# Optimization experiments

Hardware: AMD Instinct MI355X
Metric: run time of the kernel (lower is better)

The kernel has to match this reference:

```python
import jax, jax.numpy as jnp
import numpy as np

WINDOW_SIZE = 32
SIM_THRESHOLD = 0.7
N_TOKENS = 262144
DIM = 256


def setup_inputs() -> dict:
    key = jax.random.key(0)
    x = jax.random.normal(key, (N_TOKENS, DIM), dtype=jnp.float32)
    return {"x": x}


def reference(x):
    """Stage 1 (global window pruning) + Stage 3 (sequential merge) of FocusModules.

    Returns:
      mask1: [N] bool keep-mask equivalent to compute_patch_similarity's index list
             (indices retained are exactly jnp.where(mask1)[0]).
      compressed: [N, D] float, features with stage-3-dropped tokens zeroed
             (mask-compacted form of spatial_token_compression's output; the
             retained rows in order equal the torch output).
    """
    N, D = x.shape
    W = WINDOW_SIZE
    nw = N // W  # N chosen as multiple of W

    # F.normalize(x, p=2, dim=-1) with eps clamp
    norms = jnp.maximum(jnp.linalg.norm(x, axis=-1, keepdims=True), 1e-12)
    xn = x / norms

    # ---- Stage 1: per-window cosine-similarity thresholding (vectorized over windows)
    win = xn.reshape(nw, W, D)
    sim = jnp.einsum('nwd,nvd->nwv', win, win)          # [nw, W, W]
    mean_sim = sim.mean(axis=2)                          # [nw, W]
    mu = mean_sim.mean(axis=1, keepdims=True)
    sd = mean_sim.std(axis=1, ddof=1, keepdims=True)     # torch .std() is unbiased
    keep = ~(mean_sim > (mu + sd))                       # [nw, W] bool
    # fallback: if a window keeps nothing, keep its argmin token
    any_kept = keep.any(axis=1, keepdims=True)
    fallback = jnp.arange(W)[None, :] == mean_sim.argmin(axis=1)[:, None]
    keep = jnp.where(any_kept, keep, fallback)
    mask1 = keep.reshape(N)

    # ---- Stage 3: adjacent-pair cosine similarity pruning
    sim_adj = jnp.sum(xn[:-1] * xn[1:], axis=-1)         # [N-1] (unit vectors -> dot = cosine)
    mask3 = jnp.concatenate([jnp.ones((1,), dtype=bool), sim_adj < SIM_THRESHOLD])
    compressed = x * mask3[:, None].astype(x.dtype)      # zeroed instead of compacted (jit-static shape)

    return mask1, compressed
```

## Files before the change

### kernel.cpp

```cpp
#include <hip/hip_runtime.h>
#include <math.h>

#define TOKW 32
#define DIMS 256

__global__ __launch_bounds__(256) void focus_kernel(
    const float* __restrict__ x,
    float* __restrict__ out_mask,
    float* __restrict__ out_comp)
{
    const int w   = blockIdx.x;
    const int tid = threadIdx.x;
    const int tok = tid >> 3;
    const int lt  = tid & 7;

    __shared__ float sh_xn[TOKW][DIMS];
    __shared__ float sh_prev[DIMS];
    __shared__ float sh_s[DIMS];
    __shared__ float sh_m[TOKW];

    const long long g0 = (long long)w * TOKW;
    const long long tokbase = (g0 + tok) * (DIMS / 4);
    const float4* xv = (const float4*)x;

    float4 v[8];
#pragma unroll
    for (int j = 0; j < 8; ++j)
        v[j] = xv[tokbase + lt + 8 * j];

    float ss = 0.f;
#pragma unroll
    for (int j = 0; j < 8; ++j)
        ss += v[j].x * v[j].x + v[j].y * v[j].y + v[j].z * v[j].z + v[j].w * v[j].w;
    ss += __shfl_xor(ss, 1);
    ss += __shfl_xor(ss, 2);
    ss += __shfl_xor(ss, 4);
    const float rn = 1.0f / fmaxf(sqrtf(ss), 1e-12f);

#pragma unroll
    for (int j = 0; j < 8; ++j) {
        float4 n4 = make_float4(v[j].x * rn, v[j].y * rn, v[j].z * rn, v[j].w * rn);
        *(float4*)&sh_xn[tok][4 * (lt + 8 * j)] = n4;
    }

    if (tid < 64) {
        float4 pv = make_float4(0.f, 0.f, 0.f, 0.f);
        if (w > 0) pv = xv[(g0 - 1) * (DIMS / 4) + tid];
        float ps = pv.x * pv.x + pv.y * pv.y + pv.z * pv.z + pv.w * pv.w;
        ps += __shfl_xor(ps, 1);
        ps += __shfl_xor(ps, 2);
        ps += __shfl_xor(ps, 4);
        ps += __shfl_xor(ps, 8);
        ps += __shfl_xor(ps, 16);
        ps += __shfl_xor(ps, 32);
        const float prn = 1.0f / fmaxf(sqrtf(ps), 1e-12f);
        *(float4*)&sh_prev[tid * 4] =
            make_float4(pv.x * prn, pv.y * prn, pv.z * prn, pv.w * prn);
    }

    __syncthreads();

    {
        float acc = 0.f;
#pragma unroll
        for (int t = 0; t < TOKW; ++t)
            acc += sh_xn[t][tid];
        sh_s[tid] = acc;
    }
    __syncthreads();

    {
        float dp = 0.f;
#pragma unroll
        for (int j = 0; j < 8; ++j) {
            float4 s4 = *(const float4*)&sh_s[4 * (lt + 8 * j)];
            dp += v[j].x * s4.x + v[j].y * s4.y + v[j].z * s4.z + v[j].w * s4.w;
        }
        dp += __shfl_xor(dp, 1);
        dp += __shfl_xor(dp, 2);
        dp += __shfl_xor(dp, 4);
        if (lt == 0) sh_m[tok] = dp * rn * (1.0f / 32.0f);
    }
    __syncthreads();

    float mu = 0.f;
#pragma unroll
    for (int t = 0; t < TOKW; ++t)
        mu += sh_m[t];
    mu *= (1.0f / 32.0f);

    float var = 0.f;
#pragma unroll
    for (int t = 0; t < TOKW; ++t) {
        float d = sh_m[t] - mu;
        var += d * d;
    }
    var *= (1.0f / 31.0f);
    const float thr = mu + sqrtf(var);

    int cnt = 0, amin = 0;
    float mmin = sh_m[0];
#pragma unroll
    for (int t = 0; t < TOKW; ++t) {
        float m = sh_m[t];
        cnt += (m <= thr) ? 1 : 0;
        if (m < mmin) { mmin = m; amin = t; }
    }

    if (tid < TOKW) {
        bool k = (cnt > 0) ? (sh_m[tid] <= thr) : (tid == amin);
        out_mask[g0 + tid] = k ? 1.0f : 0.0f;
    }

    const float* prevrow = (tok == 0) ? sh_prev : sh_xn[tok - 1];
    float ap = 0.f;
#pragma unroll
    for (int j = 0; j < 8; ++j) {
        float4 p4 = *(const float4*)&prevrow[4 * (lt + 8 * j)];
        ap += v[j].x * p4.x + v[j].y * p4.y + v[j].z * p4.z + v[j].w * p4.w;
    }
    ap += __shfl_xor(ap, 1);
    ap += __shfl_xor(ap, 2);
    ap += __shfl_xor(ap, 4);
    const float sim_adj = ap * rn;
    const float mult = (sim_adj < 0.7f) ? 1.0f : 0.0f;

    float4* ov = (float4*)out_comp;
#pragma unroll
    for (int j = 0; j < 8; ++j)
        ov[tokbase + lt + 8 * j] =
            make_float4(v[j].x * mult, v[j].y * mult, v[j].z * mult, v[j].w * mult);
}

extern "C" void kernel_launch(void* const* d_in, const int* in_sizes, int n_in,
                              void* d_out, int out_size, void* d_ws, size_t ws_size,
                              hipStream_t stream) {
    const float* x = (const float*)d_in[0];
    const int ND = in_sizes[0];
    const int N  = ND / DIMS;
    const int nw = N / TOKW;

    float* out_mask = (float*)d_out;
    float* out_comp = out_mask + N;

    focus_kernel<<<nw, 256, 0, stream>>>(x, out_mask, out_comp);
}
```

Before: 436.0 us.

## Replace shared-memory window staging with wave shuffles and nontemporal stores

```diff
diff --git a/kernel.cpp b/kernel.cpp
--- a/kernel.cpp
+++ b/kernel.cpp
@@ -3,20 +3,24 @@
 
 #define TOKW 32
 #define DIMS 256
+
+typedef float f4v __attribute__((ext_vector_type(4)));
 
 __global__ __launch_bounds__(256) void focus_kernel(
     const float* __restrict__ x,
     float* __restrict__ out_mask,
     float* __restrict__ out_comp)
 {
-    const int w   = blockIdx.x;
-    const int tid = threadIdx.x;
-    const int tok = tid >> 3;
-    const int lt  = tid & 7;
-
-    __shared__ float sh_xn[TOKW][DIMS];
-    __shared__ float sh_prev[DIMS];
-    __shared__ float sh_s[DIMS];
+    const int tid  = threadIdx.x;
+    const int w    = blockIdx.x;
+    const int tok  = tid >> 3;
+    const int lt   = tid & 7;
+    const int wid  = tid >> 6;
+    const int tw   = tok & 7;
+    const int lane = tid & 63;
+
+    __shared__ float sh_ws[4][DIMS];
+    __shared__ float sh_bd[5][DIMS];
     __shared__ float sh_m[TOKW];
 
     const long long g0 = (long long)w * TOKW;
@@ -27,6 +31,9 @@
 #pragma unroll
     for (int j = 0; j < 8; ++j)
         v[j] = xv[tokbase + lt + 8 * j];
+
+    float4 pv = make_float4(0.f, 0.f, 0.f, 0.f);
+    if (tid < 64 && w > 0) pv = xv[(g0 - 1) * (DIMS / 4) + tid];
 
     float ss = 0.f;
 #pragma unroll
@@ -37,15 +44,47 @@
     ss += __shfl_xor(ss, 4);
     const float rn = 1.0f / fmaxf(sqrtf(ss), 1e-12f);
 
-#pragma unroll
-    for (int j = 0; j < 8; ++j) {
-        float4 n4 = make_float4(v[j].x * rn, v[j].y * rn, v[j].z * rn, v[j].w * rn);
-        *(float4*)&sh_xn[tok][4 * (lt + 8 * j)] = n4;
+    float4 t[8];
+#pragma unroll
+    for (int j = 0; j < 8; ++j) {
+        t[j].x = v[j].x * rn; t[j].y = v[j].y * rn;
+        t[j].z = v[j].z * rn; t[j].w = v[j].w * rn;
+    }
+
+    if (tw == 7) {
+#pragma unroll
+        for (int j = 0; j < 8; ++j)
+            *(float4*)&sh_bd[wid][4 * (lt + 8 * j)] = t[j];
+    }
+
+#pragma unroll
+    for (int j = 0; j < 8; ++j) {
+        t[j].x += __shfl_xor(t[j].x, 8);
+        t[j].y += __shfl_xor(t[j].y, 8);
+        t[j].z += __shfl_xor(t[j].z, 8);
+        t[j].w += __shfl_xor(t[j].w, 8);
+    }
+#pragma unroll
+    for (int j = 0; j < 8; ++j) {
+        t[j].x += __shfl_xor(t[j].x, 16);
+        t[j].y += __shfl_xor(t[j].y, 16);
+        t[j].z += __shfl_xor(t[j].z, 16);
+        t[j].w += __shfl_xor(t[j].w, 16);
+    }
+#pragma unroll
+    for (int j = 0; j < 8; ++j) {
+        t[j].x += __shfl_xor(t[j].x, 32);
+        t[j].y += __shfl_xor(t[j].y, 32);
+        t[j].z += __shfl_xor(t[j].z, 32);
+        t[j].w += __shfl_xor(t[j].w, 32);
+    }
+    if (tw == 0) {
+#pragma unroll
+        for (int j = 0; j < 8; ++j)
+            *(float4*)&sh_ws[wid][4 * (lt + 8 * j)] = t[j];
     }
 
     if (tid < 64) {
-        float4 pv = make_float4(0.f, 0.f, 0.f, 0.f);
-        if (w > 0) pv = xv[(g0 - 1) * (DIMS / 4) + tid];
         float ps = pv.x * pv.x + pv.y * pv.y + pv.z * pv.z + pv.w * pv.w;
         ps += __shfl_xor(ps, 1);
         ps += __shfl_xor(ps, 2);
@@ -54,45 +93,67 @@
         ps += __shfl_xor(ps, 16);
         ps += __shfl_xor(ps, 32);
         const float prn = 1.0f / fmaxf(sqrtf(ps), 1e-12f);
-        *(float4*)&sh_prev[tid * 4] =
+        *(float4*)&sh_bd[4][tid * 4] =
             make_float4(pv.x * prn, pv.y * prn, pv.z * prn, pv.w * prn);
     }
 
-    __syncthreads();
-
-    {
-        float acc = 0.f;
-#pragma unroll
-        for (int t = 0; t < TOKW; ++t)
-            acc += sh_xn[t][tid];
-        sh_s[tid] = acc;
-    }
     __syncthreads();
 
     {
         float dp = 0.f;
 #pragma unroll
         for (int j = 0; j < 8; ++j) {
-            float4 s4 = *(const float4*)&sh_s[4 * (lt + 8 * j)];
-            dp += v[j].x * s4.x + v[j].y * s4.y + v[j].z * s4.z + v[j].w * s4.w;
+            const int f = 4 * (lt + 8 * j);
+            const float4 s0 = *(const float4*)&sh_ws[0][f];
+            const float4 s1 = *(const float4*)&sh_ws[1][f];
+            const float4 s2 = *(const float4*)&sh_ws[2][f];
+            const float4 s3 = *(const float4*)&sh_ws[3][f];
+            dp += v[j].x * (s0.x + s1.x + s2.x + s3.x)
+                + v[j].y * (s0.y + s1.y + s2.y + s3.y)
+                + v[j].z * (s0.z + s1.z + s2.z + s3.z)
+                + v[j].w * (s0.w + s1.w + s2.w + s3.w);
         }
         dp += __shfl_xor(dp, 1);
         dp += __shfl_xor(dp, 2);
         dp += __shfl_xor(dp, 4);
         if (lt == 0) sh_m[tok] = dp * rn * (1.0f / 32.0f);
     }
+
+    const float prn_s = __shfl(rn, (lane - 8) & 63);
+    float ap = 0.f;
+#pragma unroll
+    for (int j = 0; j < 8; ++j) {
+        const float px = __shfl(v[j].x, (lane - 8) & 63);
+        const float py = __shfl(v[j].y, (lane - 8) & 63);
+        const float pz = __shfl(v[j].z, (lane - 8) & 63);
+        const float pw = __shfl(v[j].w, (lane - 8) & 63);
+        ap += px * v[j].x + py * v[j].y + pz * v[j].z + pw * v[j].w;
+    }
+    float pscale = prn_s;
+
     __syncthreads();
 
+    if (tw == 0) {
+        const float* prow = (tok == 0) ? sh_bd[4] : sh_bd[wid - 1];
+        ap = 0.f;
+#pragma unroll
+        for (int j = 0; j < 8; ++j) {
+            const float4 p4 = *(const float4*)&prow[4 * (lt + 8 * j)];
+            ap += p4.x * v[j].x + p4.y * v[j].y + p4.z * v[j].z + p4.w * v[j].w;
+        }
+        pscale = 1.0f;
+    }
+
     float mu = 0.f;
 #pragma unroll
-    for (int t = 0; t < TOKW; ++t)
-        mu += sh_m[t];
+    for (int ti = 0; ti < TOKW; ++ti)
+        mu += sh_m[ti];
     mu *= (1.0f / 32.0f);
 
     float var = 0.f;
 #pragma unroll
-    for (int t = 0; t < TOKW; ++t) {
-        float d = sh_m[t] - mu;
+    for (int ti = 0; ti < TOKW; ++ti) {
+        float d = sh_m[ti] - mu;
         var += d * d;
     }
     var *= (1.0f / 31.0f);
@@ -101,35 +162,32 @@
     int cnt = 0, amin = 0;
     float mmin = sh_m[0];
 #pragma unroll
-    for (int t = 0; t < TOKW; ++t) {
-        float m = sh_m[t];
+    for (int ti = 0; ti < TOKW; ++ti) {
+        float m = sh_m[ti];
         cnt += (m <= thr) ? 1 : 0;
-        if (m < mmin) { mmin = m; amin = t; }
+        if (m < mmin) { mmin = m; amin = ti; }
     }
 
     if (tid < TOKW) {
         bool k = (cnt > 0) ? (sh_m[tid] <= thr) : (tid == amin);
-        out_mask[g0 + tid] = k ? 1.0f : 0.0f;
-    }
-
-    const float* prevrow = (tok == 0) ? sh_prev : sh_xn[tok - 1];
-    float ap = 0.f;
-#pragma unroll
-    for (int j = 0; j < 8; ++j) {
-        float4 p4 = *(const float4*)&prevrow[4 * (lt + 8 * j)];
-        ap += v[j].x * p4.x + v[j].y * p4.y + v[j].z * p4.z + v[j].w * p4.w;
-    }
-    ap += __shfl_xor(ap, 1);
-    ap += __shfl_xor(ap, 2);
-    ap += __shfl_xor(ap, 4);
-    const float sim_adj = ap * rn;
-    const float mult = (sim_adj < 0.7f) ? 1.0f : 0.0f;
-
-    float4* ov = (float4*)out_comp;
-#pragma unroll
-    for (int j = 0; j < 8; ++j)
-        ov[tokbase + lt + 8 * j] =
-            make_float4(v[j].x * mult, v[j].y * mult, v[j].z * mult, v[j].w * mult);
+        __builtin_nontemporal_store(k ? 1.0f : 0.0f, out_mask + g0 + tid);
+    }
+
+    float sim = ap;
+    sim += __shfl_xor(sim, 1);
+    sim += __shfl_xor(sim, 2);
+    sim += __shfl_xor(sim, 4);
+    sim *= rn * pscale;
+    const float mult = (sim < 0.7f) ? 1.0f : 0.0f;
+
+    f4v* ov = (f4v*)out_comp;
+#pragma unroll
+    for (int j = 0; j < 8; ++j) {
+        f4v o;
+        o.x = v[j].x * mult; o.y = v[j].y * mult;
+        o.z = v[j].z * mult; o.w = v[j].w * mult;
+        __builtin_nontemporal_store(o, ov + tokbase + lt + 8 * j);
+    }
 }
 
 extern "C" void kernel_launch(void* const* d_in, const int* in_sizes, int n_in,
```

Measured after the change: 451.5 us. +3.6%, slower.

## Process one window per wavefront with shuffle reductions, dropping shared memory

Applied to the files above, without the earlier changes.

```diff
diff --git a/kernel.cpp b/kernel.cpp
--- a/kernel.cpp
+++ b/kernel.cpp
@@ -3,133 +3,108 @@
 
 #define TOKW 32
 #define DIMS 256
+#define F4PT (DIMS / 4)
 
-__global__ __launch_bounds__(256) void focus_kernel(
+__global__ __launch_bounds__(256, 4) void focus_kernel(
     const float* __restrict__ x,
     float* __restrict__ out_mask,
     float* __restrict__ out_comp)
 {
-    const int w   = blockIdx.x;
-    const int tid = threadIdx.x;
-    const int tok = tid >> 3;
-    const int lt  = tid & 7;
+    const int tid  = threadIdx.x;
+    const int lane = tid & 63;
+    const int win  = blockIdx.x * 4 + (tid >> 6);
 
-    __shared__ float sh_xn[TOKW][DIMS];
-    __shared__ float sh_prev[DIMS];
-    __shared__ float sh_s[DIMS];
-    __shared__ float sh_m[TOKW];
+    const long long t0 = (long long)win * TOKW;
+    const long long b4 = t0 * F4PT;
+    const float4* xv = (const float4*)x;
+    float4* ov = (float4*)out_comp;
 
-    const long long g0 = (long long)w * TOKW;
-    const long long tokbase = (g0 + tok) * (DIMS / 4);
-    const float4* xv = (const float4*)x;
+    float4 rp = make_float4(0.f, 0.f, 0.f, 0.f);
+    if (win > 0) rp = xv[b4 - F4PT + lane];
 
-    float4 v[8];
+    float4 q[4];
+    q[0] = xv[b4 + 0 * F4PT + lane];
+    q[1] = xv[b4 + 1 * F4PT + lane];
+    q[2] = xv[b4 + 2 * F4PT + lane];
+    q[3] = xv[b4 + 3 * F4PT + lane];
+
+    float ssp = rp.x * rp.x + rp.y * rp.y + rp.z * rp.z + rp.w * rp.w;
 #pragma unroll
-    for (int j = 0; j < 8; ++j)
-        v[j] = xv[tokbase + lt + 8 * j];
+    for (int mm = 1; mm < 64; mm <<= 1) ssp += __shfl_xor(ssp, mm);
+    float rn_prev = 1.0f / fmaxf(sqrtf(ssp), 1e-12f);
 
-    float ss = 0.f;
-#pragma unroll
-    for (int j = 0; j < 8; ++j)
-        ss += v[j].x * v[j].x + v[j].y * v[j].y + v[j].z * v[j].z + v[j].w * v[j].w;
-    ss += __shfl_xor(ss, 1);
-    ss += __shfl_xor(ss, 2);
-    ss += __shfl_xor(ss, 4);
-    const float rn = 1.0f / fmaxf(sqrtf(ss), 1e-12f);
+    float4 s = make_float4(0.f, 0.f, 0.f, 0.f);
+    float rn[TOKW];
+    unsigned int simbits = 0;
 
 #pragma unroll
-    for (int j = 0; j < 8; ++j) {
-        float4 n4 = make_float4(v[j].x * rn, v[j].y * rn, v[j].z * rn, v[j].w * rn);
-        *(float4*)&sh_xn[tok][4 * (lt + 8 * j)] = n4;
+    for (int j = 0; j < TOKW; ++j) {
+        const float4 rc = q[j & 3];
+        if (j + 4 < TOKW) q[j & 3] = xv[b4 + (j + 4) * F4PT + lane];
+
+        float ss = rc.x * rc.x + rc.y * rc.y + rc.z * rc.z + rc.w * rc.w;
+        float dd = rc.x * rp.x + rc.y * rp.y + rc.z * rp.z + rc.w * rp.w;
+#pragma unroll
+        for (int mm = 1; mm < 64; mm <<= 1) {
+            ss += __shfl_xor(ss, mm);
+            dd += __shfl_xor(dd, mm);
+        }
+        const float r = 1.0f / fmaxf(sqrtf(ss), 1e-12f);
+        rn[j] = r;
+        const float sim = dd * r * rn_prev;
+        if (sim < 0.7f) simbits |= (1u << j);
+        s.x += rc.x * r; s.y += rc.y * r; s.z += rc.z * r; s.w += rc.w * r;
+        rn_prev = r;
+        rp = rc;
     }
 
-    if (tid < 64) {
-        float4 pv = make_float4(0.f, 0.f, 0.f, 0.f);
-        if (w > 0) pv = xv[(g0 - 1) * (DIMS / 4) + tid];
-        float ps = pv.x * pv.x + pv.y * pv.y + pv.z * pv.z + pv.w * pv.w;
-        ps += __shfl_xor(ps, 1);
-        ps += __shfl_xor(ps, 2);
-        ps += __shfl_xor(ps, 4);
-        ps += __shfl_xor(ps, 8);
-        ps += __shfl_xor(ps, 16);
-        ps += __shfl_xor(ps, 32);
-        const float prn = 1.0f / fmaxf(sqrtf(ps), 1e-12f);
-        *(float4*)&sh_prev[tid * 4] =
-            make_float4(pv.x * prn, pv.y * prn, pv.z * prn, pv.w * prn);
+    q[0] = xv[b4 + 0 * F4PT + lane];
+    q[1] = xv[b4 + 1 * F4PT + lane];
+    q[2] = xv[b4 + 2 * F4PT + lane];
+    q[3] = xv[b4 + 3 * F4PT + lane];
+
+    float m[TOKW];
+    float mlane = 0.f;
+#pragma unroll
+    for (int j = 0; j < TOKW; ++j) {
+        const float4 rc = q[j & 3];
+        if (j + 4 < TOKW) q[j & 3] = xv[b4 + (j + 4) * F4PT + lane];
+
+        float dp = rc.x * s.x + rc.y * s.y + rc.z * s.z + rc.w * s.w;
+#pragma unroll
+        for (int mm = 1; mm < 64; mm <<= 1) dp += __shfl_xor(dp, mm);
+        const float mj = dp * rn[j] * (1.0f / 32.0f);
+        m[j] = mj;
+        if (lane == j) mlane = mj;
+
+        const float mult = ((simbits >> j) & 1u) ? 1.0f : 0.0f;
+        ov[b4 + j * F4PT + lane] =
+            make_float4(rc.x * mult, rc.y * mult, rc.z * mult, rc.w * mult);
     }
-
-    __syncthreads();
-
-    {
-        float acc = 0.f;
-#pragma unroll
-        for (int t = 0; t < TOKW; ++t)
-            acc += sh_xn[t][tid];
-        sh_s[tid] = acc;
-    }
-    __syncthreads();
-
-    {
-        float dp = 0.f;
-#pragma unroll
-        for (int j = 0; j < 8; ++j) {
-            float4 s4 = *(const float4*)&sh_s[4 * (lt + 8 * j)];
-            dp += v[j].x * s4.x + v[j].y * s4.y + v[j].z * s4.z + v[j].w * s4.w;
-        }
-        dp += __shfl_xor(dp, 1);
-        dp += __shfl_xor(dp, 2);
-        dp += __shfl_xor(dp, 4);
-        if (lt == 0) sh_m[tok] = dp * rn * (1.0f / 32.0f);
-    }
-    __syncthreads();
 
     float mu = 0.f;
 #pragma unroll
-    for (int t = 0; t < TOKW; ++t)
-        mu += sh_m[t];
+    for (int t = 0; t < TOKW; ++t) mu += m[t];
     mu *= (1.0f / 32.0f);
 
     float var = 0.f;
 #pragma unroll
-    for (int t = 0; t < TOKW; ++t) {
-        float d = sh_m[t] - mu;
-        var += d * d;
-    }
+    for (int t = 0; t < TOKW; ++t) { float d = m[t] - mu; var += d * d; }
     var *= (1.0f / 31.0f);
     const float thr = mu + sqrtf(var);
 
     int cnt = 0, amin = 0;
-    float mmin = sh_m[0];
+    float mmin = m[0];
 #pragma unroll
     for (int t = 0; t < TOKW; ++t) {
-        float m = sh_m[t];
-        cnt += (m <= thr) ? 1 : 0;
-        if (m < mmin) { mmin = m; amin = t; }
+        cnt += (m[t] <= thr) ? 1 : 0;
+        if (m[t] < mmin) { mmin = m[t]; amin = t; }
     }
 
-    if (tid < TOKW) {
-        bool k = (cnt > 0) ? (sh_m[tid] <= thr) : (tid == amin);
-        out_mask[g0 + tid] = k ? 1.0f : 0.0f;
+    if (lane < TOKW) {
+        const bool k = (cnt > 0) ? (mlane <= thr) : (lane == amin);
+        out_mask[t0 + lane] = k ? 1.0f : 0.0f;
     }
-
-    const float* prevrow = (tok == 0) ? sh_prev : sh_xn[tok - 1];
-    float ap = 0.f;
-#pragma unroll
-    for (int j = 0; j < 8; ++j) {
-        float4 p4 = *(const float4*)&prevrow[4 * (lt + 8 * j)];
-        ap += v[j].x * p4.x + v[j].y * p4.y + v[j].z * p4.z + v[j].w * p4.w;
-    }
-    ap += __shfl_xor(ap, 1);
-    ap += __shfl_xor(ap, 2);
-    ap += __shfl_xor(ap, 4);
-    const float sim_adj = ap * rn;
-    const float mult = (sim_adj < 0.7f) ? 1.0f : 0.0f;
-
-    float4* ov = (float4*)out_comp;
-#pragma unroll
-    for (int j = 0; j < 8; ++j)
-        ov[tokbase + lt + 8 * j] =
-            make_float4(v[j].x * mult, v[j].y * mult, v[j].z * mult, v[j].w * mult);
 }
 
 extern "C" void kernel_launch(void* const* d_in, const int* in_sizes, int n_in,
@@ -139,9 +114,10 @@
     const int ND = in_sizes[0];
     const int N  = ND / DIMS;
     const int nw = N / TOKW;
+    const int nb = nw / 4;
 
     float* out_mask = (float*)d_out;
     float* out_comp = out_mask + N;
 
-    focus_kernel<<<nw, 256, 0, stream>>>(x, out_mask, out_comp);
+    focus_kernel<<<nb, 256, 0, stream>>>(x, out_mask, out_comp);
 }
```

After: 681.9 us. 1.56x slower.
